# Kernel optimization log

Hardware: AMD Instinct MI355X
Metric: run time of the kernel (lower is better)

Reference implementation:

```python
import jax, jax.numpy as jnp
import numpy as np

# Ragged per-tensor sequence lengths (dim 1 of each input)
_LENS = [64, 128, 192, 256, 320, 384, 448, 512]
_B = 512   # batch size
_D = 128   # feature dim


def setup_inputs() -> dict:
    key = jax.random.key(0)
    keys = jax.random.split(key, len(_LENS))
    return {
        f"x{i}": jax.random.normal(keys[i], (_B, L, _D), dtype=jnp.float32)
        for i, L in enumerate(_LENS)
    }


def reference(x0, x1, x2, x3, x4, x5, x6, x7) -> jnp.ndarray:
    # Fused sum-over-seq + concat: equivalent to
    # torch.cat([t.sum(dim=1, keepdim=True) for t in inputs], dim=1)
    # (keep_dims=True, cat_axis=1 path -> mlu_triton_fuse_sum_cat_3d).
    inputs = (x0, x1, x2, x3, x4, x5, x6, x7)
    # Each summand is [B, 1, D]; output is [B, N, D] with N = len(inputs).
    return jnp.concatenate([t.sum(axis=1, keepdims=True) for t in inputs], axis=1)
```

## Files before the change

### kernel.cpp

```cpp
#include <hip/hip_runtime.h>
#include <hip/hip_bf16.h>


struct SumCatArgs {
    const float* x[8];
    int L[8];
};

__global__ __launch_bounds__(256) void fuse_sum_cat_kernel(
    SumCatArgs args, float* __restrict__ out) {
    const int blk = blockIdx.x;
    const int i = blk & 7;
    const int b = blk >> 3;

    const int L = args.L[i];
    const float4* __restrict__ xr =
        (const float4*)(args.x[i] + (size_t)b * (size_t)L * 128);

    const int c = threadIdx.x & 31;
    const int r = threadIdx.x >> 5;

    float4 acc0 = make_float4(0.f, 0.f, 0.f, 0.f);
    float4 acc1 = make_float4(0.f, 0.f, 0.f, 0.f);

    for (int l = r; l < L; l += 64) {
        float4 v[8];
#pragma unroll
        for (int u = 0; u < 8; ++u) {
            v[u] = xr[(size_t)(l + u * 8) * 32 + c];
        }
#pragma unroll
        for (int u = 0; u < 8; u += 2) {
            acc0.x += v[u].x; acc0.y += v[u].y;
            acc0.z += v[u].z; acc0.w += v[u].w;
            acc1.x += v[u + 1].x; acc1.y += v[u + 1].y;
            acc1.z += v[u + 1].z; acc1.w += v[u + 1].w;
        }
    }
    float4 acc = make_float4(acc0.x + acc1.x, acc0.y + acc1.y,
                             acc0.z + acc1.z, acc0.w + acc1.w);

    __shared__ float4 part[8][32];
    part[r][c] = acc;
    __syncthreads();

    if (threadIdx.x < 32) {
        float4 s = part[0][c];
#pragma unroll
        for (int k = 1; k < 8; ++k) {
            float4 v = part[k][c];
            s.x += v.x; s.y += v.y; s.z += v.z; s.w += v.w;
        }
        float4* orow = (float4*)(out + ((size_t)b * 8 + i) * 128);
        orow[c] = s;
    }
}

extern "C" void kernel_launch(void* const* d_in, const int* in_sizes, int n_in,
                              void* d_out, int out_size, void* d_ws, size_t ws_size,
                              hipStream_t stream) {
    (void)d_ws; (void)ws_size; (void)out_size;

    SumCatArgs args;
    for (int i = 0; i < 8; ++i) {
        args.x[i] = (const float*)d_in[i];
        args.L[i] = in_sizes[i] / (512 * 128);
    }

    const int n_blocks = 512 * 8;
    fuse_sum_cat_kernel<<<n_blocks, 256, 0, stream>>>(args, (float*)d_out);
}
```

Measured before the change: 508.1 us.

## Assign one wavefront per (batch, tensor) row with paired ragged lengths

```diff
diff --git a/kernel.cpp b/kernel.cpp
--- a/kernel.cpp
+++ b/kernel.cpp
@@ -1,5 +1,4 @@
 #include <hip/hip_runtime.h>
-#include <hip/hip_bf16.h>
 
 
 struct SumCatArgs {
@@ -9,57 +8,54 @@
 
 __global__ __launch_bounds__(256) void fuse_sum_cat_kernel(
     SumCatArgs args, float* __restrict__ out) {
-    const int blk = blockIdx.x;
-    const int i = blk & 7;
-    const int b = blk >> 3;
+    const int wid  = threadIdx.x >> 6;
+    const int lane = threadIdx.x & 63;
 
-    const int L = args.L[i];
+    const int bk = blockIdx.x;
+    const int b  = bk >> 1;
+    const int p  = (bk & 1) * 2 + (wid >> 1);
+    const int i  = (wid & 1) ? (7 - p) : p;
+    const int L  = args.L[i];
+
     const float4* __restrict__ xr =
-        (const float4*)(args.x[i] + (size_t)b * (size_t)L * 128);
+        (const float4*)args.x[i] + (size_t)b * (size_t)L * 32;
 
-    const int c = threadIdx.x & 31;
-    const int r = threadIdx.x >> 5;
+    float4 a0 = make_float4(0.f, 0.f, 0.f, 0.f);
+    float4 a1 = make_float4(0.f, 0.f, 0.f, 0.f);
 
-    float4 acc0 = make_float4(0.f, 0.f, 0.f, 0.f);
-    float4 acc1 = make_float4(0.f, 0.f, 0.f, 0.f);
-
-    for (int l = r; l < L; l += 64) {
+    for (int lb = 0; lb < L; lb += 16) {
+        const float4* __restrict__ w = xr + (size_t)lb * 32;
         float4 v[8];
 #pragma unroll
-        for (int u = 0; u < 8; ++u) {
-            v[u] = xr[(size_t)(l + u * 8) * 32 + c];
-        }
+        for (int u = 0; u < 8; ++u) v[u] = w[u * 64 + lane];
 #pragma unroll
         for (int u = 0; u < 8; u += 2) {
-            acc0.x += v[u].x; acc0.y += v[u].y;
-            acc0.z += v[u].z; acc0.w += v[u].w;
-            acc1.x += v[u + 1].x; acc1.y += v[u + 1].y;
-            acc1.z += v[u + 1].z; acc1.w += v[u + 1].w;
+            a0.x += v[u].x;     a0.y += v[u].y;
+            a0.z += v[u].z;     a0.w += v[u].w;
+            a1.x += v[u + 1].x; a1.y += v[u + 1].y;
+            a1.z += v[u + 1].z; a1.w += v[u + 1].w;
         }
     }
-    float4 acc = make_float4(acc0.x + acc1.x, acc0.y + acc1.y,
-                             acc0.z + acc1.z, acc0.w + acc1.w);
 
-    __shared__ float4 part[8][32];
-    part[r][c] = acc;
-    __syncthreads();
+    float4 acc = make_float4(a0.x + a1.x, a0.y + a1.y,
+                             a0.z + a1.z, a0.w + a1.w);
 
-    if (threadIdx.x < 32) {
-        float4 s = part[0][c];
-#pragma unroll
-        for (int k = 1; k < 8; ++k) {
-            float4 v = part[k][c];
-            s.x += v.x; s.y += v.y; s.z += v.z; s.w += v.w;
-        }
-        float4* orow = (float4*)(out + ((size_t)b * 8 + i) * 128);
-        orow[c] = s;
+    acc.x += __shfl_down(acc.x, 32, 64);
+    acc.y += __shfl_down(acc.y, 32, 64);
+    acc.z += __shfl_down(acc.z, 32, 64);
+    acc.w += __shfl_down(acc.w, 32, 64);
+
+    if (lane < 32) {
+        float4* __restrict__ orow =
+            (float4*)(out + ((size_t)b * 8 + i) * 128);
+        orow[lane] = acc;
     }
 }
 
 extern "C" void kernel_launch(void* const* d_in, const int* in_sizes, int n_in,
                               void* d_out, int out_size, void* d_ws, size_t ws_size,
                               hipStream_t stream) {
-    (void)d_ws; (void)ws_size; (void)out_size;
+    (void)d_ws; (void)ws_size; (void)out_size; (void)n_in;
 
     SumCatArgs args;
     for (int i = 0; i < 8; ++i) {
@@ -67,6 +63,5 @@
         args.L[i] = in_sizes[i] / (512 * 128);
     }
 
-    const int n_blocks = 512 * 8;
-    fuse_sum_cat_kernel<<<n_blocks, 256, 0, stream>>>(args, (float*)d_out);
+    fuse_sum_cat_kernel<<<1024, 256, 0, stream>>>(args, (float*)d_out);
 }
```

Measured after the change: 485.6 us. 1.05x faster.
